# Performance work log

Hardware: AMD Instinct MI355X
Metric: run time of the kernel (lower is better)

## Reference

```python
import jax, jax.numpy as jnp
import numpy as np

LATENT, INPUT, CLUSTER, N_UNITS = 1024, 512, 256, 100
N_TRAJ, N_TP = 512, 64
# minimum_step = interval/(3*N_TP); uniform spacing dt=1 => n_intermediate_tp = max(2, int(3*N_TP/(N_TP-1))) = 3
N_INTER = 3


def setup_inputs() -> dict:
    key = jax.random.key(0)
    ks = jax.random.split(key, 10)
    d = LATENT + INPUT
    w = lambda k, shp: jax.random.normal(k, shp, jnp.float32) * (shp[0] ** -0.5)
    return {
        "data": jax.random.normal(ks[0], (N_TRAJ, N_TP, INPUT), jnp.float32),
        "time_steps": jnp.arange(N_TP, dtype=jnp.float32),
        "W_u": w(ks[1], (d, LATENT)), "b_u": jnp.zeros((LATENT,), jnp.float32),
        "W_r": w(ks[2], (d, LATENT)), "b_r": jnp.zeros((LATENT,), jnp.float32),
        "W_n": w(ks[3], (d, LATENT)), "b_n": jnp.zeros((LATENT,), jnp.float32),
        "W1": w(ks[4], (LATENT, N_UNITS)), "b1": jnp.zeros((N_UNITS,), jnp.float32),
        "W2": w(ks[5], (N_UNITS, LATENT)), "b2": jnp.zeros((LATENT,), jnp.float32),
        "We": w(ks[6], (LATENT, CLUSTER)), "be": jnp.zeros((CLUSTER,), jnp.float32),
    }


def reference(data, time_steps, W_u, b_u, W_r, b_r, W_n, b_n, W1, b1, W2, b2, We, be):
    # data: [n_traj, n_tp, input]; time_steps: [n_tp]
    def gru_update(y, x):
        yc = jnp.concatenate([y, x], -1)                      # [1, n_traj, latent+input]
        u = jax.nn.sigmoid(yc @ W_u + b_u)                    # update gate
        r = jax.nn.sigmoid(yc @ W_r + b_r)                    # reset gate
        n = jnp.concatenate([y * r, x], -1) @ W_n + b_n       # new state (no nonlinearity in source)
        return (1.0 - u) * n + u * y

    def ode_f(h):
        return jnp.tanh(h @ W1 + b1) @ W2 + b2

    def step(h, inp):
        xi, dt = inp                                          # xi: [1, n_traj, input], dt scalar
        yi_ode = gru_update(h, xi)
        sub = dt / (N_INTER - 1)                              # Euler over linspace(prev_t, t_i, N_INTER)
        def euler(y, _):
            return y + ode_f(y) * sub, None
        y_end, _ = jax.lax.scan(euler, yi_ode, None, length=N_INTER - 1)
        prob = jax.nn.softmax(y_end @ We + be, -1)            # emit_probs
        return y_end, (prob, y_end)

    xs = (jnp.swapaxes(data, 0, 1)[:-1][:, None],             # [n_tp-1, 1, n_traj, input]
          time_steps[1:] - time_steps[:-1])                   # [n_tp-1]
    h0 = jnp.zeros((1, data.shape[0], LATENT), data.dtype)
    _, (probs, states) = jax.lax.scan(step, h0, xs)
    latent_ys = jnp.swapaxes(probs, 0, 1)                     # [1, n_tp-1, n_traj, cluster]
    latent_y_states = jnp.swapaxes(states, 0, 1)              # [1, n_tp-1, n_traj, latent]
    return (latent_ys, latent_y_states)
```

## Files before the change

### kernel.cpp

```cpp
#include <hip/hip_runtime.h>


typedef __bf16 bf16_t;
typedef __bf16 bf16x8 __attribute__((ext_vector_type(8)));
typedef float  f32x4  __attribute__((ext_vector_type(4)));

#define BM 64
#define BN 64
#define BK 64
#define LDT 72

__device__ __forceinline__ float sigmoidf_(float x) { return 1.f / (1.f + expf(-x)); }

__device__ __forceinline__ void split3(float v, bf16_t& h, bf16_t& m, bf16_t& l) {
  h = (bf16_t)v; float r1 = v - (float)h;
  m = (bf16_t)r1; float r2 = r1 - (float)m;
  l = (bf16_t)r2;
}

__device__ __forceinline__ void loadf8(const void* p, size_t idx, int isf32, float out[8]) {
  if (isf32) {
    const float* q = (const float*)p + idx;
    f32x4 a = *(const f32x4*)q;
    f32x4 b = *(const f32x4*)(q + 4);
    out[0]=a[0]; out[1]=a[1]; out[2]=a[2]; out[3]=a[3];
    out[4]=b[0]; out[5]=b[1]; out[6]=b[2]; out[7]=b[3];
  } else {
    bf16x8 v = *(const bf16x8*)((const bf16_t*)p + idx);
#pragma unroll
    for (int i = 0; i < 8; i++) out[i] = (float)v[i];
  }
}
__device__ __forceinline__ float loadf(const void* p, int idx, int isf32) {
  return isf32 ? ((const float*)p)[idx] : (float)((const bf16_t*)p)[idx];
}

__global__ void k_probe(const unsigned int* ts_raw, int* flag) {
  *flag = (ts_raw[0] == 0u) ? 1 : 0;
}

template<bool CATX>
__device__ __forceinline__ void gemm6(
    const bf16_t* __restrict__ Ah, const bf16_t* __restrict__ Am, const bf16_t* __restrict__ Al,
    int lda,
    const void* __restrict__ X, int isf32, int t,
    const bf16_t* __restrict__ Bh, const bf16_t* __restrict__ Bm, const bf16_t* __restrict__ Bl,
    int K,
    f32x4 acc[2][2])
{
  __shared__ __align__(16) bf16_t As[3][BM * LDT];
  __shared__ __align__(16) bf16_t Bs[3][BN * LDT];

  const int tid  = threadIdx.x;
  const int srow = tid >> 2;
  const int sc   = (tid & 3) << 4;
  const int mBase = blockIdx.y * BM;
  const int nBase = blockIdx.x * BN;
  const int arow = mBase + srow;
  const int brow = nBase + srow;

  const int lane = tid & 63;
  const int wid  = tid >> 6;
  const int wm   = (wid & 1) * 32;
  const int wn   = (wid >> 1) * 32;
  const int q8   = (lane >> 4) << 3;
  const int l16  = lane & 15;

  f32x4 z = {0.f, 0.f, 0.f, 0.f};
#pragma unroll
  for (int i = 0; i < 2; i++)
#pragma unroll
    for (int j = 0; j < 2; j++) acc[i][j] = z;

  bf16x8 pA[3][2], pB[3][2];

  auto loadA = [&](int k0) {
    int gk = k0 + sc;
    if (CATX && gk >= 1024) {
      size_t off = (size_t)arow * 32768 + (size_t)t * 512 + (size_t)(gk - 1024);
      float v[16];
      loadf8(X, off,     isf32, v);
      loadf8(X, off + 8, isf32, v + 8);
#pragma unroll
      for (int u8 = 0; u8 < 2; u8++)
#pragma unroll
        for (int j = 0; j < 8; j++) {
          bf16_t h, m, l; split3(v[u8 * 8 + j], h, m, l);
          pA[0][u8][j] = h; pA[1][u8][j] = m; pA[2][u8][j] = l;
        }
    } else {
      size_t off = (size_t)arow * lda + gk;
      pA[0][0] = *(const bf16x8*)(Ah + off); pA[0][1] = *(const bf16x8*)(Ah + off + 8);
      pA[1][0] = *(const bf16x8*)(Am + off); pA[1][1] = *(const bf16x8*)(Am + off + 8);
      pA[2][0] = *(const bf16x8*)(Al + off); pA[2][1] = *(const bf16x8*)(Al + off + 8);
    }
  };
  auto loadB = [&](int k0) {
    size_t off = (size_t)brow * K + k0 + sc;
    pB[0][0] = *(const bf16x8*)(Bh + off); pB[0][1] = *(const bf16x8*)(Bh + off + 8);
    pB[1][0] = *(const bf16x8*)(Bm + off); pB[1][1] = *(const bf16x8*)(Bm + off + 8);
    pB[2][0] = *(const bf16x8*)(Bl + off); pB[2][1] = *(const bf16x8*)(Bl + off + 8);
  };

  loadA(0); loadB(0);

  for (int k0 = 0; k0 < K; k0 += BK) {
    const int wrow = srow * LDT + sc;
#pragma unroll
    for (int p = 0; p < 3; p++) {
      *(bf16x8*)&As[p][wrow]     = pA[p][0];
      *(bf16x8*)&As[p][wrow + 8] = pA[p][1];
      *(bf16x8*)&Bs[p][wrow]     = pB[p][0];
      *(bf16x8*)&Bs[p][wrow + 8] = pB[p][1];
    }
    __syncthreads();

    if (k0 + BK < K) { loadA(k0 + BK); loadB(k0 + BK); }

#pragma unroll
    for (int kk = 0; kk < BK; kk += 32) {
      bf16x8 a[2][3], b[2][3];
#pragma unroll
      for (int p = 0; p < 3; p++) {
        a[0][p] = *(const bf16x8*)&As[p][(wm +      l16) * LDT + kk + q8];
        a[1][p] = *(const bf16x8*)&As[p][(wm + 16 + l16) * LDT + kk + q8];
        b[0][p] = *(const bf16x8*)&Bs[p][(wn +      l16) * LDT + kk + q8];
        b[1][p] = *(const bf16x8*)&Bs[p][(wn + 16 + l16) * LDT + kk + q8];
      }
#pragma unroll
      for (int mi = 0; mi < 2; mi++)
#pragma unroll
        for (int ni = 0; ni < 2; ni++) {
          f32x4 c = acc[mi][ni];
          c = __builtin_amdgcn_mfma_f32_16x16x32_bf16(a[mi][0], b[ni][0], c, 0, 0, 0);
          c = __builtin_amdgcn_mfma_f32_16x16x32_bf16(a[mi][0], b[ni][1], c, 0, 0, 0);
          c = __builtin_amdgcn_mfma_f32_16x16x32_bf16(a[mi][1], b[ni][0], c, 0, 0, 0);
          c = __builtin_amdgcn_mfma_f32_16x16x32_bf16(a[mi][1], b[ni][1], c, 0, 0, 0);
          c = __builtin_amdgcn_mfma_f32_16x16x32_bf16(a[mi][0], b[ni][2], c, 0, 0, 0);
          c = __builtin_amdgcn_mfma_f32_16x16x32_bf16(a[mi][2], b[ni][0], c, 0, 0, 0);
          acc[mi][ni] = c;
        }
    }
    __syncthreads();
  }
}

#define EPI_COORDS \
  const int lane = threadIdx.x & 63; \
  const int wid  = threadIdx.x >> 6; \
  const int row0 = blockIdx.y * BM + (wid & 1) * 32 + ((lane >> 4) << 2); \
  const int col0 = blockIdx.x * BN + (wid >> 1) * 32 + (lane & 15);

__global__ __launch_bounds__(256, 1) void k_gates(
    const bf16_t* __restrict__ hAh, const bf16_t* __restrict__ hAm, const bf16_t* __restrict__ hAl,
    const float* __restrict__ hAf,
    const void* __restrict__ data, int t,
    const bf16_t* __restrict__ Wh, const bf16_t* __restrict__ Wm, const bf16_t* __restrict__ Wl,
    const void* __restrict__ bu, const void* __restrict__ br,
    float* __restrict__ u_f32,
    bf16_t* __restrict__ hrh, bf16_t* __restrict__ hrm, bf16_t* __restrict__ hrl,
    const int* __restrict__ flg)
{
  const int isf32 = *flg;
  f32x4 acc[2][2];
  gemm6<true>(hAh, hAm, hAl, 1024, data, isf32, t, Wh, Wm, Wl, 1536, acc);
  EPI_COORDS
#pragma unroll
  for (int mi = 0; mi < 2; mi++)
#pragma unroll
    for (int ni = 0; ni < 2; ni++)
#pragma unroll
      for (int r = 0; r < 4; r++) {
        int m = row0 + mi * 16 + r;
        int n = col0 + ni * 16;
        float v = acc[mi][ni][r];
        if (n < 1024) {
          u_f32[m * 1024 + n] = sigmoidf_(v + loadf(bu, n, isf32));
        } else {
          int nn = n - 1024;
          float rr = sigmoidf_(v + loadf(br, nn, isf32));
          float hv = hAf[m * 1024 + nn] * rr;
          bf16_t h, mm_, l; split3(hv, h, mm_, l);
          int idx = m * 1024 + nn;
          hrh[idx] = h; hrm[idx] = mm_; hrl[idx] = l;
        }
      }
}

__global__ __launch_bounds__(256, 1) void k_cand(
    const bf16_t* __restrict__ hrh, const bf16_t* __restrict__ hrm, const bf16_t* __restrict__ hrl,
    const void* __restrict__ data, int t,
    const bf16_t* __restrict__ Wh, const bf16_t* __restrict__ Wm, const bf16_t* __restrict__ Wl,
    const void* __restrict__ bn,
    const float* __restrict__ u_f32, const float* __restrict__ h_f32,
    float* __restrict__ h1f,
    bf16_t* __restrict__ h1h, bf16_t* __restrict__ h1m, bf16_t* __restrict__ h1l,
    const int* __restrict__ flg)
{
  const int isf32 = *flg;
  f32x4 acc[2][2];
  gemm6<true>(hrh, hrm, hrl, 1024, data, isf32, t, Wh, Wm, Wl, 1536, acc);
  EPI_COORDS
#pragma unroll
  for (int mi = 0; mi < 2; mi++)
#pragma unroll
    for (int ni = 0; ni < 2; ni++)
#pragma unroll
      for (int r = 0; r < 4; r++) {
        int m = row0 + mi * 16 + r;
        int n = col0 + ni * 16;
        int idx = m * 1024 + n;
        float nv = acc[mi][ni][r] + loadf(bn, n, isf32);
        float u = u_f32[idx];
        float h1 = (1.f - u) * nv + u * h_f32[idx];
        h1 = fminf(fmaxf(h1, -1e6f), 1e6f);
        h1f[idx] = h1;
        bf16_t h, mm_, l; split3(h1, h, mm_, l);
        h1h[idx] = h; h1m[idx] = mm_; h1l[idx] = l;
      }
}

__global__ __launch_bounds__(256, 1) void k_tanh(
    const bf16_t* __restrict__ hh, const bf16_t* __restrict__ hm, const bf16_t* __restrict__ hl,
    const bf16_t* __restrict__ Wh, const bf16_t* __restrict__ Wm, const bf16_t* __restrict__ Wl,
    const void* __restrict__ b1,
    bf16_t* __restrict__ th, bf16_t* __restrict__ tm, bf16_t* __restrict__ tl,
    const int* __restrict__ flg)
{
  const int isf32 = *flg;
  f32x4 acc[2][2];
  gemm6<false>(hh, hm, hl, 1024, nullptr, 0, 0, Wh, Wm, Wl, 1024, acc);
  EPI_COORDS
#pragma unroll
  for (int mi = 0; mi < 2; mi++)
#pragma unroll
    for (int ni = 0; ni < 2; ni++)
#pragma unroll
      for (int r = 0; r < 4; r++) {
        int m = row0 + mi * 16 + r;
        int n = col0 + ni * 16;
        float b = (n < 100) ? loadf(b1, n, isf32) : 0.f;
        float tv = tanhf(acc[mi][ni][r] + b);
        bf16_t h, mm_, l; split3(tv, h, mm_, l);
        int idx = m * 128 + n;
        th[idx] = h; tm[idx] = mm_; tl[idx] = l;
      }
}

template<bool WRITE_STATES>
__global__ __launch_bounds__(256, 1) void k_euler(
    const bf16_t* __restrict__ th, const bf16_t* __restrict__ tm, const bf16_t* __restrict__ tl,
    const bf16_t* __restrict__ Wh, const bf16_t* __restrict__ Wm, const bf16_t* __restrict__ Wl,
    const void* __restrict__ b2, const void* __restrict__ ts, int t,
    const float* __restrict__ hprev_f32,
    float* __restrict__ houtf,
    bf16_t* __restrict__ houth, bf16_t* __restrict__ houtm, bf16_t* __restrict__ houtl,
    float* __restrict__ states, const int* __restrict__ flg)
{
  const int isf32 = *flg;
  f32x4 acc[2][2];
  gemm6<false>(th, tm, tl, 128, nullptr, 0, 0, Wh, Wm, Wl, 128, acc);
  float dt = loadf(ts, t + 1, isf32) - loadf(ts, t, isf32);
  float s = 0.5f * dt;
  EPI_COORDS
#pragma unroll
  for (int mi = 0; mi < 2; mi++)
#pragma unroll
    for (int ni = 0; ni < 2; ni++)
#pragma unroll
      for (int r = 0; r < 4; r++) {
        int m = row0 + mi * 16 + r;
        int n = col0 + ni * 16;
        int idx = m * 1024 + n;
        float hv = hprev_f32[idx] + s * (acc[mi][ni][r] + loadf(b2, n, isf32));
        hv = fminf(fmaxf(hv, -1e6f), 1e6f);
        houtf[idx] = hv;
        bf16_t h, mm_, l; split3(hv, h, mm_, l);
        houth[idx] = h; houtm[idx] = mm_; houtl[idx] = l;
        if (WRITE_STATES)
          states[((size_t)t * 512 + m) * 1024 + n] = hv;
      }
}

__global__ __launch_bounds__(256, 1) void k_emit(
    const bf16_t* __restrict__ hh, const bf16_t* __restrict__ hm, const bf16_t* __restrict__ hl,
    const bf16_t* __restrict__ Wh, const bf16_t* __restrict__ Wm, const bf16_t* __restrict__ Wl,
    const void* __restrict__ be, float* __restrict__ logits, const int* __restrict__ flg)
{
  const int isf32 = *flg;
  f32x4 acc[2][2];
  gemm6<false>(hh, hm, hl, 1024, nullptr, 0, 0, Wh, Wm, Wl, 1024, acc);
  EPI_COORDS
#pragma unroll
  for (int mi = 0; mi < 2; mi++)
#pragma unroll
    for (int ni = 0; ni < 2; ni++)
#pragma unroll
      for (int r = 0; r < 4; r++) {
        int m = row0 + mi * 16 + r;
        int n = col0 + ni * 16;
        logits[m * 256 + n] = acc[mi][ni][r] + loadf(be, n, isf32);
      }
}

__global__ __launch_bounds__(256) void k_softmax(
    const float* __restrict__ logits, float* __restrict__ probs, int t)
{
  int m = blockIdx.x;
  int j = threadIdx.x;
  float v = logits[m * 256 + j];
  __shared__ float red[256];
  red[j] = v;
  __syncthreads();
  for (int s = 128; s > 0; s >>= 1) {
    if (j < s) red[j] = fmaxf(red[j], red[j + s]);
    __syncthreads();
  }
  float mx = red[0];
  __syncthreads();
  float e = expf(v - mx);
  red[j] = e;
  __syncthreads();
  for (int s = 128; s > 0; s >>= 1) {
    if (j < s) red[j] += red[j + s];
    __syncthreads();
  }
  probs[((size_t)t * 512 + m) * 256 + j] = e / red[0];
}

__global__ void k_transpose_split(const void* __restrict__ src,
                                  bf16_t* __restrict__ dh, bf16_t* __restrict__ dm,
                                  bf16_t* __restrict__ dl,
                                  int K, int N, int Kpad, const int* __restrict__ flg)
{
  const int isf32 = *flg;
  int k = blockIdx.x * 256 + threadIdx.x;
  if (k >= Kpad) return;
  int n = blockIdx.y;
  float v = 0.f;
  if (k < K && n < N) v = loadf(src, k * N + n, isf32);
  bf16_t h, m, l; split3(v, h, m, l);
  size_t idx = (size_t)n * Kpad + k;
  dh[idx] = h; dm[idx] = m; dl[idx] = l;
}

extern "C" void kernel_launch(void* const* d_in, const int* in_sizes, int n_in,
                              void* d_out, int out_size, void* d_ws, size_t ws_size,
                              hipStream_t stream) {
  const void* data = d_in[0];
  const void* ts   = d_in[1];
  const void* Wu   = d_in[2];
  const void* bu   = d_in[3];
  const void* Wr   = d_in[4];
  const void* br   = d_in[5];
  const void* Wn   = d_in[6];
  const void* bn   = d_in[7];
  const void* W1   = d_in[8];
  const void* b1   = d_in[9];
  const void* W2   = d_in[10];
  const void* b2   = d_in[11];
  const void* We   = d_in[12];
  const void* be   = d_in[13];

  float* out_probs  = (float*)d_out;
  float* out_states = (float*)d_out + (size_t)63 * 512 * 256;

  char* p = (char*)d_ws;
  auto carve = [&](size_t bytes) { char* r = p; p += (bytes + 255) & ~255ull; return (void*)r; };
  int*    flg   = (int*)carve(256);
  bf16_t* WurTh = (bf16_t*)carve((size_t)2048 * 1536 * 2);
  bf16_t* WurTm = (bf16_t*)carve((size_t)2048 * 1536 * 2);
  bf16_t* WurTl = (bf16_t*)carve((size_t)2048 * 1536 * 2);
  bf16_t* WnTh  = (bf16_t*)carve((size_t)1024 * 1536 * 2);
  bf16_t* WnTm  = (bf16_t*)carve((size_t)1024 * 1536 * 2);
  bf16_t* WnTl  = (bf16_t*)carve((size_t)1024 * 1536 * 2);
  bf16_t* W1Th  = (bf16_t*)carve((size_t)128 * 1024 * 2);
  bf16_t* W1Tm  = (bf16_t*)carve((size_t)128 * 1024 * 2);
  bf16_t* W1Tl  = (bf16_t*)carve((size_t)128 * 1024 * 2);
  bf16_t* W2Th  = (bf16_t*)carve((size_t)1024 * 128 * 2);
  bf16_t* W2Tm  = (bf16_t*)carve((size_t)1024 * 128 * 2);
  bf16_t* W2Tl  = (bf16_t*)carve((size_t)1024 * 128 * 2);
  bf16_t* WeTh  = (bf16_t*)carve((size_t)256 * 1024 * 2);
  bf16_t* WeTm  = (bf16_t*)carve((size_t)256 * 1024 * 2);
  bf16_t* WeTl  = (bf16_t*)carve((size_t)256 * 1024 * 2);
  float*  P0f = (float*)carve((size_t)512 * 1024 * 4);
  float*  P1f = (float*)carve((size_t)512 * 1024 * 4);
  float*  P2f = (float*)carve((size_t)512 * 1024 * 4);
  bf16_t* P0h = (bf16_t*)carve((size_t)512 * 1024 * 2);
  bf16_t* P0m = (bf16_t*)carve((size_t)512 * 1024 * 2);
  bf16_t* P0l = (bf16_t*)carve((size_t)512 * 1024 * 2);
  bf16_t* P1h = (bf16_t*)carve((size_t)512 * 1024 * 2);
  bf16_t* P1m = (bf16_t*)carve((size_t)512 * 1024 * 2);
  bf16_t* P1l = (bf16_t*)carve((size_t)512 * 1024 * 2);
  bf16_t* P2h = (bf16_t*)carve((size_t)512 * 1024 * 2);
  bf16_t* P2m = (bf16_t*)carve((size_t)512 * 1024 * 2);
  bf16_t* P2l = (bf16_t*)carve((size_t)512 * 1024 * 2);
  bf16_t* HRh = (bf16_t*)carve((size_t)512 * 1024 * 2);
  bf16_t* HRm = (bf16_t*)carve((size_t)512 * 1024 * 2);
  bf16_t* HRl = (bf16_t*)carve((size_t)512 * 1024 * 2);
  float*  uf  = (float*)carve((size_t)512 * 1024 * 4);
  bf16_t* Th  = (bf16_t*)carve((size_t)512 * 128 * 2);
  bf16_t* Tm  = (bf16_t*)carve((size_t)512 * 128 * 2);
  bf16_t* Tl  = (bf16_t*)carve((size_t)512 * 128 * 2);
  float*  lg  = (float*)carve((size_t)512 * 256 * 4);

  (void)hipMemsetAsync(P0f, 0, (size_t)512 * 1024 * 4, stream);
  (void)hipMemsetAsync(P0h, 0, (size_t)512 * 1024 * 2, stream);
  (void)hipMemsetAsync(P0m, 0, (size_t)512 * 1024 * 2, stream);
  (void)hipMemsetAsync(P0l, 0, (size_t)512 * 1024 * 2, stream);

  dim3 b256(256);
  k_probe<<<1, 1, 0, stream>>>((const unsigned int*)ts, flg);

  k_transpose_split<<<dim3(6, 1024), b256, 0, stream>>>(Wu, WurTh, WurTm, WurTl, 1536, 1024, 1536, flg);
  k_transpose_split<<<dim3(6, 1024), b256, 0, stream>>>(Wr, WurTh + (size_t)1024 * 1536,
                                                        WurTm + (size_t)1024 * 1536,
                                                        WurTl + (size_t)1024 * 1536, 1536, 1024, 1536, flg);
  k_transpose_split<<<dim3(6, 1024), b256, 0, stream>>>(Wn, WnTh, WnTm, WnTl, 1536, 1024, 1536, flg);
  k_transpose_split<<<dim3(4, 128),  b256, 0, stream>>>(W1, W1Th, W1Tm, W1Tl, 1024, 100, 1024, flg);
  k_transpose_split<<<dim3(1, 1024), b256, 0, stream>>>(W2, W2Th, W2Tm, W2Tl, 100, 1024, 128, flg);
  k_transpose_split<<<dim3(4, 256),  b256, 0, stream>>>(We, WeTh, WeTm, WeTl, 1024, 256, 1024, flg);

  for (int t = 0; t < 63; t++) {
    k_gates<<<dim3(32, 8), b256, 0, stream>>>(P0h, P0m, P0l, P0f, data, t,
                                              WurTh, WurTm, WurTl, bu, br,
                                              uf, HRh, HRm, HRl, flg);
    k_cand <<<dim3(16, 8), b256, 0, stream>>>(HRh, HRm, HRl, data, t,
                                              WnTh, WnTm, WnTl, bn, uf, P0f,
                                              P1f, P1h, P1m, P1l, flg);
    k_tanh <<<dim3(2, 8),  b256, 0, stream>>>(P1h, P1m, P1l, W1Th, W1Tm, W1Tl, b1,
                                              Th, Tm, Tl, flg);
    k_euler<false><<<dim3(16, 8), b256, 0, stream>>>(Th, Tm, Tl, W2Th, W2Tm, W2Tl, b2, ts, t,
                                                     P1f, P2f, P2h, P2m, P2l, nullptr, flg);
    k_tanh <<<dim3(2, 8),  b256, 0, stream>>>(P2h, P2m, P2l, W1Th, W1Tm, W1Tl, b1,
                                              Th, Tm, Tl, flg);
    k_euler<true> <<<dim3(16, 8), b256, 0, stream>>>(Th, Tm, Tl, W2Th, W2Tm, W2Tl, b2, ts, t,
                                                     P2f, P0f, P0h, P0m, P0l, out_states, flg);
    k_emit <<<dim3(4, 8),  b256, 0, stream>>>(P0h, P0m, P0l, WeTh, WeTm, WeTl, be, lg, flg);
    k_softmax<<<512, b256, 0, stream>>>(lg, out_probs, t);
  }
}
```

Baseline: 11.01 ms.

## Fuse ODE Euler steps, emission GEMM and softmax into one row-block kernel

Replaces the six per-timestep launches (two tanh GEMMs, two Euler GEMMs, emit GEMM, softmax) with a single kernel. Each block owns 16 trajectory rows and keeps the fp32 hidden state in LDS across both Euler substeps and the emission, so intermediate states and logits no longer round-trip through global memory. Weights are read straight from global memory without LDS tiling. The grid shrinks to 32 blocks, so far fewer CUs are busy and each block does much more serial work.

```diff
diff --git a/kernel.cpp b/kernel.cpp
--- a/kernel.cpp
+++ b/kernel.cpp
@@ -9,6 +9,9 @@
 #define BN 64
 #define BK 64
 #define LDT 72
+#define LDT_T 136
+#define LDT_H 1036
+#define LDT_L 264
 
 __device__ __forceinline__ float sigmoidf_(float x) { return 1.f / (1.f + expf(-x)); }
 
@@ -17,6 +20,14 @@
   m = (bf16_t)r1; float r2 = r1 - (float)m;
   l = (bf16_t)r2;
 }
+
+#define CHAIN6(c, ah, am, al, bh, bm, bl) \
+  c = __builtin_amdgcn_mfma_f32_16x16x32_bf16(ah, bh, c, 0, 0, 0); \
+  c = __builtin_amdgcn_mfma_f32_16x16x32_bf16(ah, bm, c, 0, 0, 0); \
+  c = __builtin_amdgcn_mfma_f32_16x16x32_bf16(am, bh, c, 0, 0, 0); \
+  c = __builtin_amdgcn_mfma_f32_16x16x32_bf16(am, bm, c, 0, 0, 0); \
+  c = __builtin_amdgcn_mfma_f32_16x16x32_bf16(ah, bl, c, 0, 0, 0); \
+  c = __builtin_amdgcn_mfma_f32_16x16x32_bf16(al, bh, c, 0, 0, 0);
 
 __device__ __forceinline__ void loadf8(const void* p, size_t idx, int isf32, float out[8]) {
   if (isf32) {
@@ -132,12 +143,7 @@
 #pragma unroll
         for (int ni = 0; ni < 2; ni++) {
           f32x4 c = acc[mi][ni];
-          c = __builtin_amdgcn_mfma_f32_16x16x32_bf16(a[mi][0], b[ni][0], c, 0, 0, 0);
-          c = __builtin_amdgcn_mfma_f32_16x16x32_bf16(a[mi][0], b[ni][1], c, 0, 0, 0);
-          c = __builtin_amdgcn_mfma_f32_16x16x32_bf16(a[mi][1], b[ni][0], c, 0, 0, 0);
-          c = __builtin_amdgcn_mfma_f32_16x16x32_bf16(a[mi][1], b[ni][1], c, 0, 0, 0);
-          c = __builtin_amdgcn_mfma_f32_16x16x32_bf16(a[mi][0], b[ni][2], c, 0, 0, 0);
-          c = __builtin_amdgcn_mfma_f32_16x16x32_bf16(a[mi][2], b[ni][0], c, 0, 0, 0);
+          CHAIN6(c, a[mi][0], a[mi][1], a[mi][2], b[ni][0], b[ni][1], b[ni][2]);
           acc[mi][ni] = c;
         }
     }
@@ -220,112 +226,212 @@
       }
 }
 
-__global__ __launch_bounds__(256, 1) void k_tanh(
-    const bf16_t* __restrict__ hh, const bf16_t* __restrict__ hm, const bf16_t* __restrict__ hl,
-    const bf16_t* __restrict__ Wh, const bf16_t* __restrict__ Wm, const bf16_t* __restrict__ Wl,
-    const void* __restrict__ b1,
-    bf16_t* __restrict__ th, bf16_t* __restrict__ tm, bf16_t* __restrict__ tl,
-    const int* __restrict__ flg)
+__global__ __launch_bounds__(256, 1) void k_ode(
+    const bf16_t* __restrict__ h1h, const bf16_t* __restrict__ h1m, const bf16_t* __restrict__ h1l,
+    const float* __restrict__ h1f,
+    const bf16_t* __restrict__ W1h, const bf16_t* __restrict__ W1m, const bf16_t* __restrict__ W1l,
+    const bf16_t* __restrict__ W2h, const bf16_t* __restrict__ W2m, const bf16_t* __restrict__ W2l,
+    const bf16_t* __restrict__ Weh, const bf16_t* __restrict__ Wem, const bf16_t* __restrict__ Wel,
+    const void* __restrict__ b1, const void* __restrict__ b2, const void* __restrict__ be,
+    const void* __restrict__ ts, int t,
+    float* __restrict__ hOutf,
+    bf16_t* __restrict__ hOuth, bf16_t* __restrict__ hOutm, bf16_t* __restrict__ hOutl,
+    float* __restrict__ states, float* __restrict__ probs, const int* __restrict__ flg)
 {
+  __shared__ __align__(16) float  hS[16 * LDT_H];
+  __shared__ __align__(16) bf16_t TS[3][16 * LDT_T];
+  __shared__ __align__(16) float  lgS[16 * LDT_L];
+
+  const int tid  = threadIdx.x;
+  const int lane = tid & 63;
+  const int wid  = tid >> 6;
+  const int l16  = lane & 15;
+  const int q8   = (lane >> 4) << 3;
+  const int r0   = blockIdx.x * 16;
   const int isf32 = *flg;
-  f32x4 acc[2][2];
-  gemm6<false>(hh, hm, hl, 1024, nullptr, 0, 0, Wh, Wm, Wl, 1024, acc);
-  EPI_COORDS
-#pragma unroll
-  for (int mi = 0; mi < 2; mi++)
-#pragma unroll
-    for (int ni = 0; ni < 2; ni++)
+  const float sdt = 0.5f * (loadf(ts, t + 1, isf32) - loadf(ts, t, isf32));
+  const f32x4 z4 = {0.f, 0.f, 0.f, 0.f};
+
+#pragma unroll
+  for (int i = 0; i < 16; i++) {
+    int e = (tid + i * 256) * 4;
+    int r = e >> 10, c = e & 1023;
+    *(f32x4*)&hS[r * LDT_H + c] = *(const f32x4*)&h1f[(size_t)(r0 + r) * 1024 + c];
+  }
+
+  auto tanh_epi = [&](const f32x4& a0, const f32x4& a1) {
+#pragma unroll
+    for (int f = 0; f < 2; f++)
 #pragma unroll
       for (int r = 0; r < 4; r++) {
-        int m = row0 + mi * 16 + r;
-        int n = col0 + ni * 16;
-        float b = (n < 100) ? loadf(b1, n, isf32) : 0.f;
-        float tv = tanhf(acc[mi][ni][r] + b);
-        bf16_t h, mm_, l; split3(tv, h, mm_, l);
-        int idx = m * 128 + n;
-        th[idx] = h; tm[idx] = mm_; tl[idx] = l;
-      }
-}
-
-template<bool WRITE_STATES>
-__global__ __launch_bounds__(256, 1) void k_euler(
-    const bf16_t* __restrict__ th, const bf16_t* __restrict__ tm, const bf16_t* __restrict__ tl,
-    const bf16_t* __restrict__ Wh, const bf16_t* __restrict__ Wm, const bf16_t* __restrict__ Wl,
-    const void* __restrict__ b2, const void* __restrict__ ts, int t,
-    const float* __restrict__ hprev_f32,
-    float* __restrict__ houtf,
-    bf16_t* __restrict__ houth, bf16_t* __restrict__ houtm, bf16_t* __restrict__ houtl,
-    float* __restrict__ states, const int* __restrict__ flg)
-{
-  const int isf32 = *flg;
-  f32x4 acc[2][2];
-  gemm6<false>(th, tm, tl, 128, nullptr, 0, 0, Wh, Wm, Wl, 128, acc);
-  float dt = loadf(ts, t + 1, isf32) - loadf(ts, t, isf32);
-  float s = 0.5f * dt;
-  EPI_COORDS
-#pragma unroll
-  for (int mi = 0; mi < 2; mi++)
-#pragma unroll
-    for (int ni = 0; ni < 2; ni++)
+        int row = ((lane >> 4) << 2) + r;
+        int col = (wid << 5) + (f << 4) + l16;
+        float b = (col < 100) ? loadf(b1, col, isf32) : 0.f;
+        float tv = tanhf(((f == 0) ? a0 : a1)[r] + b);
+        bf16_t hh_, mm_, ll_; split3(tv, hh_, mm_, ll_);
+        TS[0][row * LDT_T + col] = hh_;
+        TS[1][row * LDT_T + col] = mm_;
+        TS[2][row * LDT_T + col] = ll_;
+      }
+    __syncthreads();
+  };
+
+  auto euler_stage = [&](int finalStage) {
+    f32x4 accE[16];
+#pragma unroll
+    for (int i = 0; i < 16; i++) accE[i] = z4;
+#pragma unroll
+    for (int kk = 0; kk < 128; kk += 32) {
+      bf16x8 a0 = *(const bf16x8*)&TS[0][l16 * LDT_T + kk + q8];
+      bf16x8 a1 = *(const bf16x8*)&TS[1][l16 * LDT_T + kk + q8];
+      bf16x8 a2 = *(const bf16x8*)&TS[2][l16 * LDT_T + kk + q8];
+#pragma unroll
+      for (int nf = 0; nf < 16; nf++) {
+        size_t bo = (size_t)((wid << 8) + (nf << 4) + l16) * 128 + kk + q8;
+        bf16x8 b0 = *(const bf16x8*)(W2h + bo);
+        bf16x8 b1v = *(const bf16x8*)(W2m + bo);
+        bf16x8 b2v = *(const bf16x8*)(W2l + bo);
+        CHAIN6(accE[nf], a0, a1, a2, b0, b1v, b2v);
+      }
+    }
+#pragma unroll
+    for (int nf = 0; nf < 16; nf++)
 #pragma unroll
       for (int r = 0; r < 4; r++) {
-        int m = row0 + mi * 16 + r;
-        int n = col0 + ni * 16;
-        int idx = m * 1024 + n;
-        float hv = hprev_f32[idx] + s * (acc[mi][ni][r] + loadf(b2, n, isf32));
+        int row = ((lane >> 4) << 2) + r;
+        int col = (wid << 8) + (nf << 4) + l16;
+        float hv = hS[row * LDT_H + col] + sdt * (accE[nf][r] + loadf(b2, col, isf32));
         hv = fminf(fmaxf(hv, -1e6f), 1e6f);
-        houtf[idx] = hv;
-        bf16_t h, mm_, l; split3(hv, h, mm_, l);
-        houth[idx] = h; houtm[idx] = mm_; houtl[idx] = l;
-        if (WRITE_STATES)
-          states[((size_t)t * 512 + m) * 1024 + n] = hv;
-      }
-}
-
-__global__ __launch_bounds__(256, 1) void k_emit(
-    const bf16_t* __restrict__ hh, const bf16_t* __restrict__ hm, const bf16_t* __restrict__ hl,
-    const bf16_t* __restrict__ Wh, const bf16_t* __restrict__ Wm, const bf16_t* __restrict__ Wl,
-    const void* __restrict__ be, float* __restrict__ logits, const int* __restrict__ flg)
-{
-  const int isf32 = *flg;
-  f32x4 acc[2][2];
-  gemm6<false>(hh, hm, hl, 1024, nullptr, 0, 0, Wh, Wm, Wl, 1024, acc);
-  EPI_COORDS
-#pragma unroll
-  for (int mi = 0; mi < 2; mi++)
-#pragma unroll
-    for (int ni = 0; ni < 2; ni++)
+        hS[row * LDT_H + col] = hv;
+        if (finalStage) {
+          size_t gi = (size_t)(r0 + row) * 1024 + col;
+          hOutf[gi] = hv;
+          bf16_t hh_, mm_, ll_; split3(hv, hh_, mm_, ll_);
+          hOuth[gi] = hh_; hOutm[gi] = mm_; hOutl[gi] = ll_;
+          states[((size_t)t * 512 + r0 + row) * 1024 + col] = hv;
+        }
+      }
+    __syncthreads();
+  };
+
+  auto ldA_hS = [&](bf16x8 aa[3], int k0) {
+    const float* hp = &hS[l16 * LDT_H + k0 + q8];
+    f32x4 u = *(const f32x4*)hp;
+    f32x4 v = *(const f32x4*)(hp + 4);
+    float vv[8] = {u[0], u[1], u[2], u[3], v[0], v[1], v[2], v[3]};
+#pragma unroll
+    for (int j = 0; j < 8; j++) {
+      bf16_t h, m, l; split3(vv[j], h, m, l);
+      aa[0][j] = h; aa[1][j] = m; aa[2][j] = l;
+    }
+  };
+
+  {
+    f32x4 acc0 = z4, acc1 = z4;
+    bf16x8 a[3], c0[3], c1[3], na[3], nc0[3], nc1[3];
+    auto ld = [&](bf16x8 aa[3], bf16x8 bb0[3], bf16x8 bb1[3], int k0) {
+      size_t ao = (size_t)(r0 + l16) * 1024 + k0 + q8;
+      aa[0] = *(const bf16x8*)(h1h + ao);
+      aa[1] = *(const bf16x8*)(h1m + ao);
+      aa[2] = *(const bf16x8*)(h1l + ao);
+      size_t b0o = (size_t)((wid << 5) + l16) * 1024 + k0 + q8;
+      size_t b1o = b0o + (size_t)16 * 1024;
+      bb0[0] = *(const bf16x8*)(W1h + b0o); bb0[1] = *(const bf16x8*)(W1m + b0o); bb0[2] = *(const bf16x8*)(W1l + b0o);
+      bb1[0] = *(const bf16x8*)(W1h + b1o); bb1[1] = *(const bf16x8*)(W1m + b1o); bb1[2] = *(const bf16x8*)(W1l + b1o);
+    };
+    ld(a, c0, c1, 0);
+    for (int k0 = 0; k0 < 1024; k0 += 64) {
+      ld(na, nc0, nc1, k0 + 32);
+      CHAIN6(acc0, a[0], a[1], a[2], c0[0], c0[1], c0[2]);
+      CHAIN6(acc1, a[0], a[1], a[2], c1[0], c1[1], c1[2]);
+      if (k0 + 64 < 1024) ld(a, c0, c1, k0 + 64);
+      CHAIN6(acc0, na[0], na[1], na[2], nc0[0], nc0[1], nc0[2]);
+      CHAIN6(acc1, na[0], na[1], na[2], nc1[0], nc1[1], nc1[2]);
+    }
+    tanh_epi(acc0, acc1);
+  }
+
+  euler_stage(0);
+
+  {
+    f32x4 acc0 = z4, acc1 = z4;
+    bf16x8 a[3], c0[3], c1[3], na[3], nc0[3], nc1[3];
+    auto ldB = [&](bf16x8 bb0[3], bf16x8 bb1[3], int k0) {
+      size_t b0o = (size_t)((wid << 5) + l16) * 1024 + k0 + q8;
+      size_t b1o = b0o + (size_t)16 * 1024;
+      bb0[0] = *(const bf16x8*)(W1h + b0o); bb0[1] = *(const bf16x8*)(W1m + b0o); bb0[2] = *(const bf16x8*)(W1l + b0o);
+      bb1[0] = *(const bf16x8*)(W1h + b1o); bb1[1] = *(const bf16x8*)(W1m + b1o); bb1[2] = *(const bf16x8*)(W1l + b1o);
+    };
+    ldA_hS(a, 0); ldB(c0, c1, 0);
+    for (int k0 = 0; k0 < 1024; k0 += 64) {
+      ldA_hS(na, k0 + 32); ldB(nc0, nc1, k0 + 32);
+      CHAIN6(acc0, a[0], a[1], a[2], c0[0], c0[1], c0[2]);
+      CHAIN6(acc1, a[0], a[1], a[2], c1[0], c1[1], c1[2]);
+      if (k0 + 64 < 1024) { ldA_hS(a, k0 + 64); ldB(c0, c1, k0 + 64); }
+      CHAIN6(acc0, na[0], na[1], na[2], nc0[0], nc0[1], nc0[2]);
+      CHAIN6(acc1, na[0], na[1], na[2], nc1[0], nc1[1], nc1[2]);
+    }
+    tanh_epi(acc0, acc1);
+  }
+
+  euler_stage(1);
+
+  {
+    f32x4 accL[4];
+#pragma unroll
+    for (int i = 0; i < 4; i++) accL[i] = z4;
+    bf16x8 a[3], bb[4][3], na[3], nbb[4][3];
+    auto ldB = [&](bf16x8 b[4][3], int k0) {
+#pragma unroll
+      for (int nf = 0; nf < 4; nf++) {
+        size_t bo = (size_t)((wid << 6) + (nf << 4) + l16) * 1024 + k0 + q8;
+        b[nf][0] = *(const bf16x8*)(Weh + bo);
+        b[nf][1] = *(const bf16x8*)(Wem + bo);
+        b[nf][2] = *(const bf16x8*)(Wel + bo);
+      }
+    };
+    ldA_hS(a, 0); ldB(bb, 0);
+    for (int k0 = 0; k0 < 1024; k0 += 64) {
+      ldA_hS(na, k0 + 32); ldB(nbb, k0 + 32);
+#pragma unroll
+      for (int nf = 0; nf < 4; nf++) { CHAIN6(accL[nf], a[0], a[1], a[2], bb[nf][0], bb[nf][1], bb[nf][2]); }
+      if (k0 + 64 < 1024) { ldA_hS(a, k0 + 64); ldB(bb, k0 + 64); }
+#pragma unroll
+      for (int nf = 0; nf < 4; nf++) { CHAIN6(accL[nf], na[0], na[1], na[2], nbb[nf][0], nbb[nf][1], nbb[nf][2]); }
+    }
+#pragma unroll
+    for (int nf = 0; nf < 4; nf++)
 #pragma unroll
       for (int r = 0; r < 4; r++) {
-        int m = row0 + mi * 16 + r;
-        int n = col0 + ni * 16;
-        logits[m * 256 + n] = acc[mi][ni][r] + loadf(be, n, isf32);
-      }
-}
-
-__global__ __launch_bounds__(256) void k_softmax(
-    const float* __restrict__ logits, float* __restrict__ probs, int t)
-{
-  int m = blockIdx.x;
-  int j = threadIdx.x;
-  float v = logits[m * 256 + j];
-  __shared__ float red[256];
-  red[j] = v;
-  __syncthreads();
-  for (int s = 128; s > 0; s >>= 1) {
-    if (j < s) red[j] = fmaxf(red[j], red[j + s]);
+        int row = ((lane >> 4) << 2) + r;
+        int col = (wid << 6) + (nf << 4) + l16;
+        lgS[row * LDT_L + col] = accL[nf][r] + loadf(be, col, isf32);
+      }
     __syncthreads();
   }
-  float mx = red[0];
-  __syncthreads();
-  float e = expf(v - mx);
-  red[j] = e;
-  __syncthreads();
-  for (int s = 128; s > 0; s >>= 1) {
-    if (j < s) red[j] += red[j + s];
-    __syncthreads();
-  }
-  probs[((size_t)t * 512 + m) * 256 + j] = e / red[0];
+
+  {
+    int row = tid >> 4;
+    int j   = tid & 15;
+    float mx = -3.4e38f;
+#pragma unroll
+    for (int s = 0; s < 16; s++) mx = fmaxf(mx, lgS[row * LDT_L + j + 16 * s]);
+    mx = fmaxf(mx, __shfl_xor(mx, 1));
+    mx = fmaxf(mx, __shfl_xor(mx, 2));
+    mx = fmaxf(mx, __shfl_xor(mx, 4));
+    mx = fmaxf(mx, __shfl_xor(mx, 8));
+    float e[16], sum = 0.f;
+#pragma unroll
+    for (int s = 0; s < 16; s++) { e[s] = expf(lgS[row * LDT_L + j + 16 * s] - mx); sum += e[s]; }
+    sum += __shfl_xor(sum, 1);
+    sum += __shfl_xor(sum, 2);
+    sum += __shfl_xor(sum, 4);
+    sum += __shfl_xor(sum, 8);
+    float inv = 1.f / sum;
+#pragma unroll
+    for (int s = 0; s < 16; s++)
+      probs[((size_t)t * 512 + r0 + row) * 256 + j + 16 * s] = e[s] * inv;
+  }
 }
 
 __global__ void k_transpose_split(const void* __restrict__ src,
@@ -385,24 +491,16 @@
   bf16_t* WeTl  = (bf16_t*)carve((size_t)256 * 1024 * 2);
   float*  P0f = (float*)carve((size_t)512 * 1024 * 4);
   float*  P1f = (float*)carve((size_t)512 * 1024 * 4);
-  float*  P2f = (float*)carve((size_t)512 * 1024 * 4);
   bf16_t* P0h = (bf16_t*)carve((size_t)512 * 1024 * 2);
   bf16_t* P0m = (bf16_t*)carve((size_t)512 * 1024 * 2);
   bf16_t* P0l = (bf16_t*)carve((size_t)512 * 1024 * 2);
   bf16_t* P1h = (bf16_t*)carve((size_t)512 * 1024 * 2);
   bf16_t* P1m = (bf16_t*)carve((size_t)512 * 1024 * 2);
   bf16_t* P1l = (bf16_t*)carve((size_t)512 * 1024 * 2);
-  bf16_t* P2h = (bf16_t*)carve((size_t)512 * 1024 * 2);
-  bf16_t* P2m = (bf16_t*)carve((size_t)512 * 1024 * 2);
-  bf16_t* P2l = (bf16_t*)carve((size_t)512 * 1024 * 2);
   bf16_t* HRh = (bf16_t*)carve((size_t)512 * 1024 * 2);
   bf16_t* HRm = (bf16_t*)carve((size_t)512 * 1024 * 2);
   bf16_t* HRl = (bf16_t*)carve((size_t)512 * 1024 * 2);
   float*  uf  = (float*)carve((size_t)512 * 1024 * 4);
-  bf16_t* Th  = (bf16_t*)carve((size_t)512 * 128 * 2);
-  bf16_t* Tm  = (bf16_t*)carve((size_t)512 * 128 * 2);
-  bf16_t* Tl  = (bf16_t*)carve((size_t)512 * 128 * 2);
-  float*  lg  = (float*)carve((size_t)512 * 256 * 4);
 
   (void)hipMemsetAsync(P0f, 0, (size_t)512 * 1024 * 4, stream);
   (void)hipMemsetAsync(P0h, 0, (size_t)512 * 1024 * 2, stream);
@@ -428,15 +526,12 @@
     k_cand <<<dim3(16, 8), b256, 0, stream>>>(HRh, HRm, HRl, data, t,
                                               WnTh, WnTm, WnTl, bn, uf, P0f,
                                               P1f, P1h, P1m, P1l, flg);
-    k_tanh <<<dim3(2, 8),  b256, 0, stream>>>(P1h, P1m, P1l, W1Th, W1Tm, W1Tl, b1,
-                                              Th, Tm, Tl, flg);
-    k_euler<false><<<dim3(16, 8), b256, 0, stream>>>(Th, Tm, Tl, W2Th, W2Tm, W2Tl, b2, ts, t,
-                                                     P1f, P2f, P2h, P2m, P2l, nullptr, flg);
-    k_tanh <<<dim3(2, 8),  b256, 0, stream>>>(P2h, P2m, P2l, W1Th, W1Tm, W1Tl, b1,
-                                              Th, Tm, Tl, flg);
-    k_euler<true> <<<dim3(16, 8), b256, 0, stream>>>(Th, Tm, Tl, W2Th, W2Tm, W2Tl, b2, ts, t,
-                                                     P2f, P0f, P0h, P0m, P0l, out_states, flg);
-    k_emit <<<dim3(4, 8),  b256, 0, stream>>>(P0h, P0m, P0l, WeTh, WeTm, WeTl, be, lg, flg);
-    k_softmax<<<512, b256, 0, stream>>>(lg, out_probs, t);
-  }
-}
+    k_ode  <<<32, b256, 0, stream>>>(P1h, P1m, P1l, P1f,
+                                     W1Th, W1Tm, W1Tl,
+                                     W2Th, W2Tm, W2Tl,
+                                     WeTh, WeTm, WeTl,
+                                     b1, b2, be, ts, t,
+                                     P0f, P0h, P0m, P0l,
+                                     out_states, out_probs, flg);
+  }
+}
```

Result: slower. 15.46 ms (+40.4%).
